# Kernel optimization log

Measured on AMD Instinct MI355X. Metric: run time of the kernel, lower is better.

Reference implementation:

```python
import jax, jax.numpy as jnp
import numpy as np

B, N, C = 128, 36, 1024
K_NB = 16            # neighbors per node (top-k, includes loop)
KERNEL = 8           # number of Gaussian kernels
OUT = 1024           # out_dim; per-kernel out = OUT // KERNEL
PI = np.float32(np.pi)


def setup_inputs() -> dict:
    key = jax.random.key(0)
    ks = jax.random.split(key, 9)
    node_feats = jax.random.normal(ks[0], (B, N, C), dtype=jnp.float32)
    node_centre = jax.random.uniform(ks[1], (B, N, 2), dtype=jnp.float32)
    neighbor_idx = jax.random.randint(ks[2], (B * N, K_NB), 0, B * N, dtype=jnp.int32)
    graph_weights = jax.random.uniform(ks[3], (B * N * K_NB, 1), dtype=jnp.float32)
    # Gaussian kernel params (per reset_parameters)
    mean_rho = jax.random.uniform(ks[4], (1, KERNEL), dtype=jnp.float32)
    mean_theta = jax.random.uniform(ks[5], (1, KERNEL), minval=-PI, maxval=PI, dtype=jnp.float32)
    precision_rho = jax.random.uniform(ks[6], (1, KERNEL), minval=0.5, maxval=1.0, dtype=jnp.float32)
    precision_theta = jax.random.uniform(ks[7], (1, KERNEL), minval=0.5, maxval=1.0, dtype=jnp.float32)
    # per-kernel Linear(node_dim, out_dim//kernel, bias=False), stacked: [K, d_out_k, C]
    conv_w = jax.random.normal(ks[8], (KERNEL, OUT // KERNEL, C), dtype=jnp.float32) * (1.0 / np.sqrt(C))
    return {
        "node_feats": node_feats,
        "node_centre": node_centre,
        "neighbor_idx": neighbor_idx,
        "graph_weights": graph_weights,
        "mean_rho": mean_rho,
        "mean_theta": mean_theta,
        "precision_rho": precision_rho,
        "precision_theta": precision_theta,
        "conv_w": conv_w,
    }


def _forward(node_feats, node_centre, graph_weights,
             mean_rho, mean_theta, precision_rho, precision_theta,
             conv_w, neighbor_idx):
    b, n, c = node_feats.shape
    bn = b * n
    # pseudo polar coordinates per edge: centre_i - centre_j
    centre = node_centre.reshape(bn, 2)                       # [BN, 2]
    diff = centre[:, None, :] - centre[neighbor_idx]          # [BN, K_nb, 2]
    coord_x = diff[..., 0].reshape(-1)                        # [E]
    coord_y = diff[..., 1].reshape(-1)
    rho = jnp.sqrt(coord_x ** 2 + coord_y ** 2)
    theta = jnp.arctan2(coord_x, coord_y)
    # Gaussian mixture membership weights over KERNEL kernels
    w_rho = jnp.exp(-0.5 * (rho[:, None] - mean_rho) ** 2 / (1e-14 + precision_rho ** 2))
    first_angle = jnp.abs(theta[:, None] - mean_theta)
    second_angle = jnp.abs(2.0 * PI - first_angle)
    w_theta = jnp.exp(-0.5 * jnp.minimum(first_angle, second_angle) ** 2 / (1e-14 + precision_theta ** 2))
    weights = w_rho * w_theta                                  # [E, KERNEL]
    weights = jnp.where(jnp.isnan(weights), 0.0, weights)
    weights = weights / jnp.sum(weights, axis=1, keepdims=True)
    # combine with graph edge weights
    edge_w = graph_weights * weights                           # [E, KERNEL]
    edge_w = edge_w.reshape(bn, K_NB, KERNEL).transpose(0, 2, 1)  # [BN, K, K_nb]
    # gather neighbor features and weighted aggregate (bmm)
    nbr = node_feats.reshape(bn, c)[neighbor_idx]              # [BN, K_nb, C]
    agg = jnp.einsum('ekn,enc->ekc', edge_w, nbr)              # [BN, KERNEL, C]
    agg = agg.reshape(b, n, KERNEL, c)
    # per-kernel linear then concat over kernel dim
    out = jnp.einsum('bnkc,kdc->bnkd', agg, conv_w)            # [B, N, KERNEL, OUT//KERNEL]
    out = out.reshape(b, n, -1)                                # [B, N, OUT]
    return jax.nn.relu(out)


def reference(node_feats, node_centre, neighbor_idx, graph_weights,
              mean_rho, mean_theta, precision_rho, precision_theta, conv_w):
    return _forward(node_feats, node_centre, graph_weights,
                    mean_rho, mean_theta, precision_rho, precision_theta,
                    conv_w, neighbor_idx)
```

## Files before the change

### kernel.cpp

```cpp
#include <hip/hip_runtime.h>
#include <hip/hip_bf16.h>
#include <stdint.h>

#define B_DIM   128
#define N_DIM   36
#define C_DIM   1024
#define KNB     16
#define NKER    8
#define OUTD    1024
#define BN_NODES (B_DIM * N_DIM)
#define E_EDGES  (BN_NODES * KNB)
#define PI_F 3.14159265358979323846f

typedef __attribute__((ext_vector_type(8))) short bf16x8;
typedef __attribute__((ext_vector_type(4))) float floatx4;

struct alignas(8) U16x4 { unsigned short x, y, z, w; };

__device__ __forceinline__ unsigned short f2bf(float f) {
  union { float f; uint32_t u; } v; v.f = f;
  uint32_t u = v.u;
  return (unsigned short)((u + 0x7fffu + ((u >> 16) & 1u)) >> 16);
}
__device__ __forceinline__ float bf2f(unsigned short h) {
  union { uint32_t u; float f; } v; v.u = ((uint32_t)h) << 16;
  return v.f;
}

__device__ __forceinline__ void gload16(const void* g, void* l) {
  __builtin_amdgcn_global_load_lds((__attribute__((address_space(1))) void*)(g),
                                   (__attribute__((address_space(3))) void*)(l),
                                   16, 0, 0);
}

__global__ __launch_bounds__(256)
void edge_kernel(const float* __restrict__ centre,
                 const int*   __restrict__ nbr,
                 const float* __restrict__ gw,
                 const float* __restrict__ mrho,
                 const float* __restrict__ mth,
                 const float* __restrict__ prho,
                 const float* __restrict__ pth,
                 float* __restrict__ edge_w)
{
  int e = blockIdx.x * 256 + threadIdx.x;
  if (e >= E_EDGES) return;
  int n = e >> 4;
  int j = e & 15;
  int m = nbr[e];
  float cx = centre[2 * n]     - centre[2 * m];
  float cy = centre[2 * n + 1] - centre[2 * m + 1];
  float rho   = sqrtf(cx * cx + cy * cy);
  float theta = atan2f(cx, cy);

  float w[NKER];
  float sum = 0.f;
#pragma unroll
  for (int k = 0; k < NKER; ++k) {
    float dr = rho - mrho[k];
    float pr = prho[k];
    float wr = expf(-0.5f * dr * dr / (1e-14f + pr * pr));
    float fa = fabsf(theta - mth[k]);
    float sa = fabsf(2.0f * PI_F - fa);
    float mm = fminf(fa, sa);
    float pt = pth[k];
    float wt = expf(-0.5f * mm * mm / (1e-14f + pt * pt));
    float ww = wr * wt;
    w[k] = (ww != ww) ? 0.f : ww;
    sum += w[k];
  }
  float scale = gw[e] / sum;
#pragma unroll
  for (int k = 0; k < NKER; ++k)
    edge_w[(n * NKER + k) * KNB + j] = w[k] * scale;
}

__global__ __launch_bounds__(256)
void cast_kernel(const float* __restrict__ feats,
                 const float* __restrict__ cw,
                 unsigned short* __restrict__ fb,
                 unsigned short* __restrict__ wb)
{
  const int NF4 = (BN_NODES * C_DIM) / 4;
  const int NW4 = (C_DIM * OUTD) / 4;
  int tid = blockIdx.x * 256 + threadIdx.x;
  if (tid < NF4) {
    float4 v = ((const float4*)feats)[tid];
    U16x4 o = { f2bf(v.x), f2bf(v.y), f2bf(v.z), f2bf(v.w) };
    ((U16x4*)fb)[tid] = o;
  } else {
    int t = tid - NF4;
    if (t < NW4) {
      float4 v = ((const float4*)cw)[t];
      U16x4 o = { f2bf(v.x), f2bf(v.y), f2bf(v.z), f2bf(v.w) };
      ((U16x4*)wb)[t] = o;
    }
  }
}

__global__ __launch_bounds__(256)
void gemm_bt(const unsigned short* __restrict__ A,
             const unsigned short* __restrict__ Bt,
             unsigned short* __restrict__ D)
{
  __shared__ unsigned short At [128 * 32];
  __shared__ unsigned short Bts[128 * 32];

  const int tid  = threadIdx.x;
  const int lane = tid & 63;
  const int wave = tid >> 6;
  const int wr   = wave >> 1;
  const int wc   = wave & 1;
  const int row0 = blockIdx.x * 128;
  const int col0 = blockIdx.y * 128;

  floatx4 acc[4][4] = {};

  const int r0 = tid >> 2,         q0 = tid & 3;
  const int r1 = (tid + 256) >> 2; const int q1 = q0;

  const unsigned short* Ag0 = A  + (size_t)(row0 + r0) * C_DIM + q0 * 8;
  const unsigned short* Ag1 = A  + (size_t)(row0 + r1) * C_DIM + q1 * 8;
  const unsigned short* Bg0 = Bt + (size_t)(col0 + r0) * C_DIM + q0 * 8;
  const unsigned short* Bg1 = Bt + (size_t)(col0 + r1) * C_DIM + q1 * 8;
  unsigned short* la0 = &At [tid * 8];
  unsigned short* la1 = &At [(tid + 256) * 8];
  unsigned short* lb0 = &Bts[tid * 8];
  unsigned short* lb1 = &Bts[(tid + 256) * 8];

  const int qk = (lane >> 4) << 3;
  const int lr = lane & 15;

  for (int k0 = 0; k0 < C_DIM; k0 += 32) {
    gload16(Ag0 + k0, la0);
    gload16(Ag1 + k0, la1);
    gload16(Bg0 + k0, lb0);
    gload16(Bg1 + k0, lb1);
    __syncthreads();

    bf16x8 af[4], bfr[4];
#pragma unroll
    for (int i = 0; i < 4; ++i) {
      af[i]  = *(const bf16x8*)&At [(wr * 64 + i * 16 + lr) * 32 + qk];
      bfr[i] = *(const bf16x8*)&Bts[(wc * 64 + i * 16 + lr) * 32 + qk];
    }
#pragma unroll
    for (int i = 0; i < 4; ++i)
#pragma unroll
      for (int j = 0; j < 4; ++j)
        acc[i][j] = __builtin_amdgcn_mfma_f32_16x16x32_bf16(af[i], bfr[j], acc[i][j], 0, 0, 0);
    __syncthreads();
  }

  const int quad = lane >> 4;
#pragma unroll
  for (int i = 0; i < 4; ++i)
#pragma unroll
    for (int j = 0; j < 4; ++j)
#pragma unroll
      for (int r = 0; r < 4; ++r) {
        int row = row0 + wr * 64 + i * 16 + quad * 4 + r;
        int col = col0 + wc * 64 + j * 16 + lr;
        D[(size_t)row * OUTD + col] = f2bf(acc[i][j][r]);
      }
}

__global__ __launch_bounds__(256)
void agg_kernel(const unsigned short* __restrict__ proj,
                const float* __restrict__ edge_w,
                const int*   __restrict__ nbr,
                float* __restrict__ out)
{
  __shared__ float ew[NKER * KNB];
  __shared__ int   idx[KNB];
  const int n = blockIdx.x;
  const int t = threadIdx.x;
  if (t < 128)            ew[t]        = edge_w[n * 128 + t];
  else if (t < 128 + KNB) idx[t - 128] = nbr[n * KNB + (t - 128)];
  __syncthreads();

  const int k = t >> 5;
  float a0 = 0.f, a1 = 0.f, a2 = 0.f, a3 = 0.f;
#pragma unroll
  for (int j = 0; j < KNB; ++j) {
    float wv = ew[k * KNB + j];
    U16x4 v = *(const U16x4*)&proj[(size_t)idx[j] * OUTD + t * 4];
    a0 += wv * bf2f(v.x);
    a1 += wv * bf2f(v.y);
    a2 += wv * bf2f(v.z);
    a3 += wv * bf2f(v.w);
  }
  float4 r;
  r.x = fmaxf(a0, 0.f); r.y = fmaxf(a1, 0.f);
  r.z = fmaxf(a2, 0.f); r.w = fmaxf(a3, 0.f);
  ((float4*)out)[(size_t)n * (OUTD / 4) + t] = r;
}

extern "C" void kernel_launch(void* const* d_in, const int* in_sizes, int n_in,
                              void* d_out, int out_size, void* d_ws, size_t ws_size,
                              hipStream_t stream)
{
  const float* feats  = (const float*)d_in[0];
  const float* centre = (const float*)d_in[1];
  const int*   nbr    = (const int*)  d_in[2];
  const float* gw     = (const float*)d_in[3];
  const float* mrho   = (const float*)d_in[4];
  const float* mth    = (const float*)d_in[5];
  const float* prho   = (const float*)d_in[6];
  const float* pth    = (const float*)d_in[7];
  const float* cw     = (const float*)d_in[8];
  float* out = (float*)d_out;

  char* ws = (char*)d_ws;
  unsigned short* fb    = (unsigned short*)(ws);
  unsigned short* wb    = (unsigned short*)(ws + 9437184);
  unsigned short* proj  = (unsigned short*)(ws + 11534336);
  float*          edgew = (float*)         (ws + 20971520);

  edge_kernel<<<dim3(E_EDGES / 256), dim3(256), 0, stream>>>(
      centre, nbr, gw, mrho, mth, prho, pth, edgew);
  cast_kernel<<<dim3(((BN_NODES * C_DIM) / 4 + (C_DIM * OUTD) / 4) / 256), dim3(256), 0, stream>>>(
      feats, cw, fb, wb);
  gemm_bt<<<dim3(BN_NODES / 128, OUTD / 128), dim3(256), 0, stream>>>(fb, wb, proj);
  agg_kernel<<<dim3(BN_NODES), dim3(256), 0, stream>>>(proj, edgew, nbr, out);
}
```

Before: 132.2 us.

## Pipeline GEMM loads with 4-stage LDS ring and fuse edge weights into aggregation

Turns the bf16 MFMA GEMM's single-buffered K loop into a 4-stage ring of LDS buffers filled by async global-to-LDS loads. Explicit vmcnt waits and barriers let later tiles load while the current one is computed, hiding global load latency. Separately, the per-edge Gaussian weight computation is moved into the aggregation kernel, which drops one launch and the edge-weight round trip through memory. The costs are four times the LDS per block (64KB), which may lower occupancy, and extra barriers plus redundant trig work in each aggregation block.

```diff
diff --git a/kernel.cpp b/kernel.cpp
--- a/kernel.cpp
+++ b/kernel.cpp
@@ -33,47 +33,8 @@
                                    16, 0, 0);
 }
 
-__global__ __launch_bounds__(256)
-void edge_kernel(const float* __restrict__ centre,
-                 const int*   __restrict__ nbr,
-                 const float* __restrict__ gw,
-                 const float* __restrict__ mrho,
-                 const float* __restrict__ mth,
-                 const float* __restrict__ prho,
-                 const float* __restrict__ pth,
-                 float* __restrict__ edge_w)
-{
-  int e = blockIdx.x * 256 + threadIdx.x;
-  if (e >= E_EDGES) return;
-  int n = e >> 4;
-  int j = e & 15;
-  int m = nbr[e];
-  float cx = centre[2 * n]     - centre[2 * m];
-  float cy = centre[2 * n + 1] - centre[2 * m + 1];
-  float rho   = sqrtf(cx * cx + cy * cy);
-  float theta = atan2f(cx, cy);
-
-  float w[NKER];
-  float sum = 0.f;
-#pragma unroll
-  for (int k = 0; k < NKER; ++k) {
-    float dr = rho - mrho[k];
-    float pr = prho[k];
-    float wr = expf(-0.5f * dr * dr / (1e-14f + pr * pr));
-    float fa = fabsf(theta - mth[k]);
-    float sa = fabsf(2.0f * PI_F - fa);
-    float mm = fminf(fa, sa);
-    float pt = pth[k];
-    float wt = expf(-0.5f * mm * mm / (1e-14f + pt * pt));
-    float ww = wr * wt;
-    w[k] = (ww != ww) ? 0.f : ww;
-    sum += w[k];
-  }
-  float scale = gw[e] / sum;
-#pragma unroll
-  for (int k = 0; k < NKER; ++k)
-    edge_w[(n * NKER + k) * KNB + j] = w[k] * scale;
-}
+#define VMCNT(n) asm volatile("s_waitcnt vmcnt(" #n ")" ::: "memory")
+#define LGKM0()  asm volatile("s_waitcnt lgkmcnt(0)" ::: "memory")
 
 __global__ __launch_bounds__(256)
 void cast_kernel(const float* __restrict__ feats,
@@ -103,8 +64,8 @@
              const unsigned short* __restrict__ Bt,
              unsigned short* __restrict__ D)
 {
-  __shared__ unsigned short At [128 * 32];
-  __shared__ unsigned short Bts[128 * 32];
+  __shared__ unsigned short At [4][128 * 32];
+  __shared__ unsigned short Bts[4][128 * 32];
 
   const int tid  = threadIdx.x;
   const int lane = tid & 63;
@@ -116,41 +77,53 @@
 
   floatx4 acc[4][4] = {};
 
-  const int r0 = tid >> 2,         q0 = tid & 3;
-  const int r1 = (tid + 256) >> 2; const int q1 = q0;
-
-  const unsigned short* Ag0 = A  + (size_t)(row0 + r0) * C_DIM + q0 * 8;
-  const unsigned short* Ag1 = A  + (size_t)(row0 + r1) * C_DIM + q1 * 8;
-  const unsigned short* Bg0 = Bt + (size_t)(col0 + r0) * C_DIM + q0 * 8;
-  const unsigned short* Bg1 = Bt + (size_t)(col0 + r1) * C_DIM + q1 * 8;
-  unsigned short* la0 = &At [tid * 8];
-  unsigned short* la1 = &At [(tid + 256) * 8];
-  unsigned short* lb0 = &Bts[tid * 8];
-  unsigned short* lb1 = &Bts[(tid + 256) * 8];
+  const int r0 = tid >> 2, q = tid & 3;
+  const int r1 = r0 + 64;
+
+  const unsigned short* Ag0 = A  + (size_t)(row0 + r0) * C_DIM + q * 8;
+  const unsigned short* Ag1 = A  + (size_t)(row0 + r1) * C_DIM + q * 8;
+  const unsigned short* Bg0 = Bt + (size_t)(col0 + r0) * C_DIM + q * 8;
+  const unsigned short* Bg1 = Bt + (size_t)(col0 + r1) * C_DIM + q * 8;
 
   const int qk = (lane >> 4) << 3;
   const int lr = lane & 15;
 
-  for (int k0 = 0; k0 < C_DIM; k0 += 32) {
-    gload16(Ag0 + k0, la0);
-    gload16(Ag1 + k0, la1);
-    gload16(Bg0 + k0, lb0);
-    gload16(Bg1 + k0, lb1);
-    __syncthreads();
-
-    bf16x8 af[4], bfr[4];
-#pragma unroll
-    for (int i = 0; i < 4; ++i) {
-      af[i]  = *(const bf16x8*)&At [(wr * 64 + i * 16 + lr) * 32 + qk];
-      bfr[i] = *(const bf16x8*)&Bts[(wc * 64 + i * 16 + lr) * 32 + qk];
+#define STAGE(s, k0) do {                              \
+    gload16(Ag0 + (k0), &At [s][tid * 8]);             \
+    gload16(Ag1 + (k0), &At [s][(tid + 256) * 8]);     \
+    gload16(Bg0 + (k0), &Bts[s][tid * 8]);             \
+    gload16(Bg1 + (k0), &Bts[s][(tid + 256) * 8]);     \
+  } while (0)
+
+#define FRAGS(s)                                                           \
+    bf16x8 af[4], bfr[4];                                                  \
+    _Pragma("unroll") for (int i = 0; i < 4; ++i) {                        \
+      af[i]  = *(const bf16x8*)&At [s][(wr * 64 + i * 16 + lr) * 32 + qk]; \
+      bfr[i] = *(const bf16x8*)&Bts[s][(wc * 64 + i * 16 + lr) * 32 + qk]; \
     }
-#pragma unroll
-    for (int i = 0; i < 4; ++i)
-#pragma unroll
-      for (int j = 0; j < 4; ++j)
-        acc[i][j] = __builtin_amdgcn_mfma_f32_16x16x32_bf16(af[i], bfr[j], acc[i][j], 0, 0, 0);
-    __syncthreads();
-  }
+
+#define MFMAS()                                                            \
+    _Pragma("unroll") for (int i = 0; i < 4; ++i)                          \
+    _Pragma("unroll") for (int j = 0; j < 4; ++j)                          \
+      acc[i][j] = __builtin_amdgcn_mfma_f32_16x16x32_bf16(af[i], bfr[j], acc[i][j], 0, 0, 0);
+
+  STAGE(0, 0); STAGE(1, 32); STAGE(2, 64); STAGE(3, 96);
+
+#pragma unroll 4
+  for (int it = 0; it < 28; ++it) {
+    const int s = it & 3;
+    VMCNT(12);
+    __builtin_amdgcn_s_barrier();
+    FRAGS(s);
+    LGKM0();
+    __builtin_amdgcn_s_barrier();
+    STAGE(s, (it + 4) * 32);
+    MFMAS();
+  }
+  { VMCNT(12); __builtin_amdgcn_s_barrier(); FRAGS(0); MFMAS(); }
+  { VMCNT(8);  __builtin_amdgcn_s_barrier(); FRAGS(1); MFMAS(); }
+  { VMCNT(4);  __builtin_amdgcn_s_barrier(); FRAGS(2); MFMAS(); }
+  { VMCNT(0);  __builtin_amdgcn_s_barrier(); FRAGS(3); MFMAS(); }
 
   const int quad = lane >> 4;
 #pragma unroll
@@ -163,27 +136,81 @@
         int col = col0 + wc * 64 + j * 16 + lr;
         D[(size_t)row * OUTD + col] = f2bf(acc[i][j][r]);
       }
+#undef STAGE
+#undef FRAGS
+#undef MFMAS
 }
 
 __global__ __launch_bounds__(256)
-void agg_kernel(const unsigned short* __restrict__ proj,
-                const float* __restrict__ edge_w,
-                const int*   __restrict__ nbr,
-                float* __restrict__ out)
-{
-  __shared__ float ew[NKER * KNB];
+void agg_fused(const unsigned short* __restrict__ proj,
+               const float* __restrict__ centre,
+               const int*   __restrict__ nbr,
+               const float* __restrict__ gw,
+               const float* __restrict__ mrho,
+               const float* __restrict__ mth,
+               const float* __restrict__ prho,
+               const float* __restrict__ pth,
+               float* __restrict__ out)
+{
   __shared__ int   idx[KNB];
+  __shared__ float nx[KNB], ny[KNB];
+  __shared__ float cc[2];
+  __shared__ float wk[KNB][NKER];
+  __shared__ float scl[KNB];
+  __shared__ float ew[NKER][KNB];
+
   const int n = blockIdx.x;
   const int t = threadIdx.x;
-  if (t < 128)            ew[t]        = edge_w[n * 128 + t];
-  else if (t < 128 + KNB) idx[t - 128] = nbr[n * KNB + (t - 128)];
+
+  if (t < KNB) {
+    int m = nbr[n * KNB + t];
+    idx[t] = m;
+    nx[t] = centre[2 * m];
+    ny[t] = centre[2 * m + 1];
+  } else if (t == KNB) {
+    cc[0] = centre[2 * n];
+    cc[1] = centre[2 * n + 1];
+  }
+  __syncthreads();
+
+  if (t < 128) {
+    int j = t >> 3, k = t & 7;
+    float cx = cc[0] - nx[j];
+    float cy = cc[1] - ny[j];
+    float rho   = sqrtf(cx * cx + cy * cy);
+    float theta = atan2f(cx, cy);
+    float dr = rho - mrho[k];
+    float pr = prho[k];
+    float w_r = expf(-0.5f * dr * dr / (1e-14f + pr * pr));
+    float fa = fabsf(theta - mth[k]);
+    float sa = fabsf(2.0f * PI_F - fa);
+    float mm = fminf(fa, sa);
+    float pt = pth[k];
+    float w_t = expf(-0.5f * mm * mm / (1e-14f + pt * pt));
+    float ww = w_r * w_t;
+    wk[j][k] = (ww != ww) ? 0.f : ww;
+  }
+  __syncthreads();
+
+  if (t < KNB) {
+    float s = 0.f;
+#pragma unroll
+    for (int k = 0; k < NKER; ++k) s += wk[t][k];
+    scl[t] = gw[n * KNB + t] / s;
+  }
+  __syncthreads();
+
+  if (t < 128) {
+    int j = t >> 3, k = t & 7;
+    ew[k][j] = wk[j][k] * scl[j];
+  }
   __syncthreads();
 
   const int k = t >> 5;
   float a0 = 0.f, a1 = 0.f, a2 = 0.f, a3 = 0.f;
 #pragma unroll
   for (int j = 0; j < KNB; ++j) {
-    float wv = ew[k * KNB + j];
+    float wv = ew[k][j];
     U16x4 v = *(const U16x4*)&proj[(size_t)idx[j] * OUTD + t * 4];
     a0 += wv * bf2f(v.x);
     a1 += wv * bf2f(v.y);
@@ -212,15 +239,13 @@
   float* out = (float*)d_out;
 
   char* ws = (char*)d_ws;
-  unsigned short* fb    = (unsigned short*)(ws);
-  unsigned short* wb    = (unsigned short*)(ws + 9437184);
-  unsigned short* proj  = (unsigned short*)(ws + 11534336);
-  float*          edgew = (float*)         (ws + 20971520);
-
-  edge_kernel<<<dim3(E_EDGES / 256), dim3(256), 0, stream>>>(
-      centre, nbr, gw, mrho, mth, prho, pth, edgew);
-  cast_kernel<<<dim3(((BN_NODES * C_DIM) / 4 + (C_DIM * OUTD) / 4) / 256), dim3(256), 0, stream>>>(
-      feats, cw, fb, wb);
+  unsigned short* fb   = (unsigned short*)(ws);
+  unsigned short* wb   = (unsigned short*)(ws + 9437184);
+  unsigned short* proj = (unsigned short*)(ws + 11534336);
+
+  cast_kernel<<<dim3(((BN_NODES * C_DIM) / 4 + (C_DIM * OUTD) / 4) / 256),
+                dim3(256), 0, stream>>>(feats, cw, fb, wb);
   gemm_bt<<<dim3(BN_NODES / 128, OUTD / 128), dim3(256), 0, stream>>>(fb, wb, proj);
-  agg_kernel<<<dim3(BN_NODES), dim3(256), 0, stream>>>(proj, edgew, nbr, out);
-}
+  agg_fused<<<dim3(BN_NODES), dim3(256), 0, stream>>>(
+      proj, centre, nbr, gw, mrho, mth, prho, pth, out);
+}
```

Result: faster. 128.0 us (-3.2%).
